# Optimization experiments

Hardware: AMD Instinct MI355X
Metric: run time of the kernel (lower is better)

Reference implementation:

```python
import jax, jax.numpy as jnp
import numpy as np

B, T, H, L = 64, 1024, 1024, 2


def setup_inputs() -> dict:
    key = jax.random.key(0)
    ks = jax.random.split(key, 5)
    stdv = 1.0 / np.sqrt(H)
    u = lambda k, shape: jax.random.uniform(k, shape, jnp.float32, -stdv, stdv)
    return {
        "Xt": jax.random.normal(ks[0], (B, T, H), jnp.float32),
        "Wih": u(ks[1], (L, H, H)),
        "bih": u(ks[2], (L, H)),
        "Whh": u(ks[3], (L, H, H)),
        "bhh": u(ks[4], (L, H)),
    }


def reference(Xt, Wih, bih, Whh, bhh):
    # Stacked Elman RNN, batch_first, zero initial hidden state, tanh, dropout=0.
    # h: [L, B, H] stacked per-layer hidden states.
    h0 = jnp.zeros((L, B, H), Xt.dtype)

    def step(h, x_t):  # h: [L,B,H], x_t: [B,H]
        x = x_t
        new_h = []
        for i in range(L):
            x = jnp.tanh(x @ Wih[i].T + bih[i] + h[i] @ Whh[i].T + bhh[i])
            new_h.append(x)
        return jnp.stack(new_h), x  # carry new hidden, emit top-layer output

    xs = jnp.swapaxes(Xt, 0, 1)  # [T, B, H]
    hT, ys = jax.lax.scan(step, h0, xs)
    out = jnp.swapaxes(ys, 0, 1)  # [B, T, H]
    return (out, hT)
```

## Files before the change

kernel.cpp:

```cpp
#include <hip/hip_runtime.h>
#include <hip/hip_bf16.h>
#include <stdint.h>

#define HH 1024
#define BB 64
#define TT 1024

typedef __attribute__((ext_vector_type(8))) short short8;
typedef __attribute__((ext_vector_type(4))) float f32x4;

__device__ __forceinline__ unsigned short f2bf(float f) {
  union { float f; unsigned u; } v; v.f = f;
  unsigned r = v.u + 0x7fffu + ((v.u >> 16) & 1u);
  return (unsigned short)(r >> 16);
}

__device__ __forceinline__ float h2f(unsigned short u) {
  _Float16 h;
  __builtin_memcpy(&h, &u, 2);
  return (float)h;
}

__device__ __forceinline__ float ftanh(float x) {
  float e = __expf(2.0f * x);
  return 1.0f - 2.0f * __builtin_amdgcn_rcpf(e + 1.0f);
}

__global__ void prep_kernel(const float* __restrict__ Wih, const float* __restrict__ Whh,
                            const float* __restrict__ bih, const float* __restrict__ bhh,
                            unsigned short* __restrict__ wih_b, unsigned short* __restrict__ whh_b,
                            float* __restrict__ bias01) {
  int i = blockIdx.x * 256 + threadIdx.x;
  wih_b[i] = f2bf(Wih[i]);
  whh_b[i] = f2bf(Whh[i]);
  if (i < 2 * HH) bias01[i] = bih[i] + bhh[i];
}

__device__ __forceinline__ size_t rowperm(int r) {
  return ((size_t)(r & 63) << 10) | (size_t)(r >> 6);
}

template<bool ABF16, bool APERM, bool CPERM, bool OUTF16>
__global__ __launch_bounds__(256)
void gemm_bias(const void* __restrict__ Av, const unsigned short* __restrict__ Wb,
               const float* __restrict__ bias, void* __restrict__ GoutV) {
  __shared__ unsigned short As[128 * 40];
  __shared__ unsigned short Bs[128 * 40];
  const int tn = blockIdx.x & 7;
  const int tm = blockIdx.x >> 3;
  const int tid = threadIdx.x;
  const int wid = tid >> 6, lane = tid & 63;
  const int wr = (wid >> 1) * 64, wc = (wid & 1) * 64;
  const int l15 = lane & 15, l4 = lane >> 4;
  f32x4 acc[4][4] = {};

  const float* Af = (const float*)Av;
  const unsigned short* Ab = (const unsigned short*)Av;
  const int sr = tid >> 2;
  const int sk = (tid & 3) * 8;

  for (int k0 = 0; k0 < HH; k0 += 32) {
    __syncthreads();
#pragma unroll
    for (int p = 0; p < 2; ++p) {
      const int row = p * 64 + sr;
      const int rg = tm * 128 + row;
      const size_t ar = APERM ? rowperm(rg) : (size_t)rg;
      if (ABF16) {
        const unsigned short* src = Ab + ar * HH + k0 + sk;
        *(short8*)&As[row * 40 + sk] = *(const short8*)src;
      } else {
        const float* src = Af + ar * HH + k0 + sk;
        float4 x = *(const float4*)src;
        float4 y = *(const float4*)(src + 4);
        short8 v;
        v[0] = (short)f2bf(x.x); v[1] = (short)f2bf(x.y);
        v[2] = (short)f2bf(x.z); v[3] = (short)f2bf(x.w);
        v[4] = (short)f2bf(y.x); v[5] = (short)f2bf(y.y);
        v[6] = (short)f2bf(y.z); v[7] = (short)f2bf(y.w);
        *(short8*)&As[row * 40 + sk] = v;
      }
      const unsigned short* wsrc = Wb + (size_t)(tn * 128 + row) * HH + k0 + sk;
      *(short8*)&Bs[row * 40 + sk] = *(const short8*)wsrc;
    }
    __syncthreads();
    short8 a[4], b[4];
#pragma unroll
    for (int i = 0; i < 4; ++i) a[i] = *(short8*)&As[(wr + i * 16 + l15) * 40 + l4 * 8];
#pragma unroll
    for (int j = 0; j < 4; ++j) b[j] = *(short8*)&Bs[(wc + j * 16 + l15) * 40 + l4 * 8];
#pragma unroll
    for (int i = 0; i < 4; ++i)
#pragma unroll
      for (int j = 0; j < 4; ++j)
        acc[i][j] = __builtin_amdgcn_mfma_f32_16x16x32_bf16(a[i], b[j], acc[i][j], 0, 0, 0);
  }
#pragma unroll
  for (int j = 0; j < 4; ++j) {
    const int gc = tn * 128 + wc + j * 16 + l15;
    const float bv = bias[gc];
#pragma unroll
    for (int i = 0; i < 4; ++i) {
#pragma unroll
      for (int jj = 0; jj < 4; ++jj) {
        const int gr = tm * 128 + wr + i * 16 + l4 * 4 + jj;
        const size_t orow = CPERM ? rowperm(gr) : (size_t)gr;
        const float val = acc[i][j][jj] + bv;
        if (OUTF16) ((_Float16*)GoutV)[orow * HH + gc] = (_Float16)val;
        else        ((float*)GoutV)[orow * HH + gc] = val;
      }
    }
  }
}

__global__ __launch_bounds__(256)
void rec_fused(const unsigned short* __restrict__ Gh,
               const unsigned short* __restrict__ Whh0_b,
               const unsigned short* __restrict__ Wih1_b,
               const unsigned short* __restrict__ Whh1_b,
               const float* __restrict__ bias1,
               unsigned short* __restrict__ h0p,
               unsigned short* __restrict__ h1p,
               float* __restrict__ outp,
               float* __restrict__ hT,
               unsigned int* flags) {
  const int g = blockIdx.x;
  const int tid = threadIdx.x, wid = tid >> 6, lane = tid & 63;
  const int l15 = lane & 15, l4 = lane >> 4, kp = l4 * 8;
  __shared__ unsigned short Wl0[16 * 1032];
  __shared__ unsigned short Wl1[16 * 2056];

  for (int idx = tid; idx < 16 * 64; idx += 256) {
    const int j = idx >> 6, kseg = (idx & 63) * 16;
    const short8* s0 = (const short8*)&Whh0_b[(size_t)(g * 16 + j) * HH + kseg];
    *(short8*)&Wl0[j * 1032 + kseg] = s0[0];
    *(short8*)&Wl0[j * 1032 + kseg + 8] = s0[1];
    const short8* s1 = (const short8*)&Wih1_b[(size_t)(g * 16 + j) * HH + kseg];
    *(short8*)&Wl1[j * 2056 + kseg] = s1[0];
    *(short8*)&Wl1[j * 2056 + kseg + 8] = s1[1];
    const short8* s2 = (const short8*)&Whh1_b[(size_t)(g * 16 + j) * HH + kseg];
    *(short8*)&Wl1[j * 2056 + 1024 + kseg] = s2[0];
    *(short8*)&Wl1[j * 2056 + 1024 + kseg + 8] = s2[1];
  }
  __syncthreads();

  const int col = g * 16 + l15;
  const unsigned short* b0row = &Wl0[l15 * 1032 + kp];
  const unsigned short* b1row = &Wl1[l15 * 2056 + kp];
  const float bc1 = bias1[col];
  const uint64_t myflag = (uint64_t)(flags + g);
  const uint64_t pollflag = (uint64_t)(flags + lane);

  int bidx[4];
#pragma unroll
  for (int jj = 0; jj < 4; ++jj) bidx[jj] = wid * 16 + l4 * 4 + jj;

  float gv[4], gn[4];
#pragma unroll
  for (int jj = 0; jj < 4; ++jj) gv[jj] = h2f(Gh[(size_t)bidx[jj] * HH + col]);

  for (int p = 0; p <= TT; ++p) {
    if (p + 1 < TT) {
#pragma unroll
      for (int jj = 0; jj < 4; ++jj)
        gn[jj] = h2f(Gh[((size_t)(p + 1) * BB + bidx[jj]) * HH + col]);
    }

    if (p < TT) {
      f32x4 acc0 = {}, acc1 = {};
      if (p > 0) {
        const unsigned short* arow =
            h0p + ((p - 1) & 1) * (BB * HH) + (size_t)(wid * 16 + l15) * HH + kp;
#pragma unroll
        for (int ks = 0; ks < 32; ks += 2) {
          short8 a0 = *(const short8*)(arow + ks * 32);
          short8 w0 = *(const short8*)(b0row + ks * 32);
          acc0 = __builtin_amdgcn_mfma_f32_16x16x32_bf16(a0, w0, acc0, 0, 0, 0);
          short8 a1 = *(const short8*)(arow + (ks + 1) * 32);
          short8 w1 = *(const short8*)(b0row + (ks + 1) * 32);
          acc1 = __builtin_amdgcn_mfma_f32_16x16x32_bf16(a1, w1, acc1, 0, 0, 0);
        }
      }
      unsigned short* hc = h0p + (p & 1) * (BB * HH);
#pragma unroll
      for (int jj = 0; jj < 4; ++jj) {
        const float pre = acc0[jj] + acc1[jj] + gv[jj];
        const float h = ftanh(pre);
        const unsigned short hb = f2bf(h);
        const uint64_t ha = (uint64_t)(hc + (size_t)bidx[jj] * HH + col);
        asm volatile("global_store_short %0, %1, off sc0 sc1"
                     :: "v"(ha), "v"((unsigned)hb) : "memory");
        if (p == TT - 1) hT[(size_t)bidx[jj] * HH + col] = h;
      }
    }

    if (p >= 1) {
      const int t1 = p - 1;
      f32x4 acc0 = {}, acc1 = {};
      {
        const unsigned short* arow =
            h0p + (t1 & 1) * (BB * HH) + (size_t)(wid * 16 + l15) * HH + kp;
#pragma unroll
        for (int ks = 0; ks < 32; ks += 2) {
          short8 a0 = *(const short8*)(arow + ks * 32);
          short8 w0 = *(const short8*)(b1row + ks * 32);
          acc0 = __builtin_amdgcn_mfma_f32_16x16x32_bf16(a0, w0, acc0, 0, 0, 0);
          short8 a1 = *(const short8*)(arow + (ks + 1) * 32);
          short8 w1 = *(const short8*)(b1row + (ks + 1) * 32);
          acc1 = __builtin_amdgcn_mfma_f32_16x16x32_bf16(a1, w1, acc1, 0, 0, 0);
        }
      }
      if (t1 > 0) {
        const unsigned short* arow =
            h1p + ((t1 - 1) & 1) * (BB * HH) + (size_t)(wid * 16 + l15) * HH + kp;
#pragma unroll
        for (int ks = 0; ks < 32; ks += 2) {
          short8 a0 = *(const short8*)(arow + ks * 32);
          short8 w0 = *(const short8*)(b1row + 1024 + ks * 32);
          acc0 = __builtin_amdgcn_mfma_f32_16x16x32_bf16(a0, w0, acc0, 0, 0, 0);
          short8 a1 = *(const short8*)(arow + (ks + 1) * 32);
          short8 w1 = *(const short8*)(b1row + 1024 + (ks + 1) * 32);
          acc1 = __builtin_amdgcn_mfma_f32_16x16x32_bf16(a1, w1, acc1, 0, 0, 0);
        }
      }
      unsigned short* hc = h1p + (t1 & 1) * (BB * HH);
#pragma unroll
      for (int jj = 0; jj < 4; ++jj) {
        const float pre = acc0[jj] + acc1[jj] + bc1;
        const float h = ftanh(pre);
        outp[((size_t)bidx[jj] * TT + t1) * HH + col] = h;
        if (t1 < TT - 1) {
          const unsigned short hb = f2bf(h);
          const uint64_t ha = (uint64_t)(hc + (size_t)bidx[jj] * HH + col);
          asm volatile("global_store_short %0, %1, off sc0 sc1"
                       :: "v"(ha), "v"((unsigned)hb) : "memory");
        } else {
          hT[BB * HH + (size_t)bidx[jj] * HH + col] = h;
        }
      }
    }

    if (p < TT) {
      asm volatile("s_waitcnt vmcnt(0)" ::: "memory");
      __syncthreads();
      if (tid == 0) {
        const unsigned val = (unsigned)(p + 1);
        asm volatile("s_waitcnt vmcnt(0)\n\t"
                     "global_store_dword %0, %1, off sc0 sc1"
                     :: "v"(myflag), "v"(val) : "memory");
      }
      if (wid == 0) {
        const unsigned tgt = (unsigned)(p + 1);
        unsigned v;
        do {
          asm volatile("global_load_dword %0, %1, off sc0 sc1\n\t"
                       "s_waitcnt vmcnt(0)"
                       : "=v"(v) : "v"(pollflag) : "memory");
        } while (!__all((int)(v >= tgt)));
        __builtin_amdgcn_fence(__ATOMIC_ACQUIRE, "agent");
      }
      __syncthreads();
#pragma unroll
      for (int jj = 0; jj < 4; ++jj) gv[jj] = gn[jj];
    }
  }
}

extern "C" void kernel_launch(void* const* d_in, const int* in_sizes, int n_in,
                              void* d_out, int out_size, void* d_ws, size_t ws_size,
                              hipStream_t stream) {
  const float* Xt  = (const float*)d_in[0];
  const float* Wih = (const float*)d_in[1];
  const float* bih = (const float*)d_in[2];
  const float* Whh = (const float*)d_in[3];
  const float* bhh = (const float*)d_in[4];
  float* out = (float*)d_out;
  float* hT  = out + (size_t)BB * TT * HH;

  char* ws = (char*)d_ws;
  unsigned short* wih_b  = (unsigned short*)(ws);
  unsigned short* whh_b  = (unsigned short*)(ws + (4u << 20));
  float*          bias01 = (float*)(ws + (8u << 20));
  unsigned short* Gh     = (unsigned short*)(ws + (16u << 20));
  unsigned short* h0p    = (unsigned short*)(ws + (145u << 20));
  unsigned short* h1p    = (unsigned short*)(ws + (146u << 20));
  unsigned int*   flags  = (unsigned int*)(ws + (147u << 20));

  if (ws_size < (150u << 20)) return;

  hipMemsetAsync(flags, 0, 4096, stream);
  prep_kernel<<<8192, 256, 0, stream>>>(Wih, Whh, bih, bhh, wih_b, whh_b, bias01);

  gemm_bias<false, true, false, true><<<4096, 256, 0, stream>>>(Xt, wih_b, bias01, Gh);

  {
    const unsigned short* G = Gh;
    const unsigned short* W0 = whh_b;
    const unsigned short* W1i = wih_b + (size_t)HH * HH;
    const unsigned short* W1h = whh_b + (size_t)HH * HH;
    const float* b1 = bias01 + HH;
    unsigned short* p0 = h0p;
    unsigned short* p1 = h1p;
    float* op = out;
    float* ht = hT;
    unsigned int* fl = flags;
    void* args[] = {&G, &W0, &W1i, &W1h, &b1, &p0, &p1, &op, &ht, &fl};
    hipLaunchCooperativeKernel((void*)rec_fused, dim3(64), dim3(256), args, 0, stream);
  }
}
```

Before: 16.19 ms.

## Replace persistent cooperative kernel with per-timestep kernel launches

Swaps the single cooperative persistent kernel and its flag-based grid barrier for 1025 separate step-kernel launches, so the kernel boundary serves as the inter-step synchronization. Each launch reloads the weight slices from global memory into LDS. Layer-1's input product is also merged into the layer-0 loop so both share the loaded h0 fragments. The trade is dropping the spin-wait barrier in exchange for per-launch overhead and repeated weight staging at every step.

```diff
diff --git a/kernel.cpp b/kernel.cpp
--- a/kernel.cpp
+++ b/kernel.cpp
@@ -114,16 +114,18 @@
 }
 
 __global__ __launch_bounds__(256)
-void rec_fused(const unsigned short* __restrict__ Gh,
-               const unsigned short* __restrict__ Whh0_b,
-               const unsigned short* __restrict__ Wih1_b,
-               const unsigned short* __restrict__ Whh1_b,
-               const float* __restrict__ bias1,
-               unsigned short* __restrict__ h0p,
-               unsigned short* __restrict__ h1p,
-               float* __restrict__ outp,
-               float* __restrict__ hT,
-               unsigned int* flags) {
+void step_kernel(int p,
+                 const unsigned short* __restrict__ Gh,
+                 const unsigned short* __restrict__ Whh0_b,
+                 const unsigned short* __restrict__ Wih1_b,
+                 const unsigned short* __restrict__ Whh1_b,
+                 const float* __restrict__ bias1,
+                 const unsigned short* __restrict__ h0_prev,
+                 unsigned short* __restrict__ h0_cur,
+                 const unsigned short* __restrict__ h1_prev,
+                 unsigned short* __restrict__ h1_cur,
+                 float* __restrict__ outp,
+                 float* __restrict__ hT) {
   const int g = blockIdx.x;
   const int tid = threadIdx.x, wid = tid >> 6, lane = tid & 63;
   const int l15 = lane & 15, l4 = lane >> 4, kp = l4 * 8;
@@ -132,136 +134,87 @@
 
   for (int idx = tid; idx < 16 * 64; idx += 256) {
     const int j = idx >> 6, kseg = (idx & 63) * 16;
-    const short8* s0 = (const short8*)&Whh0_b[(size_t)(g * 16 + j) * HH + kseg];
-    *(short8*)&Wl0[j * 1032 + kseg] = s0[0];
-    *(short8*)&Wl0[j * 1032 + kseg + 8] = s0[1];
-    const short8* s1 = (const short8*)&Wih1_b[(size_t)(g * 16 + j) * HH + kseg];
-    *(short8*)&Wl1[j * 2056 + kseg] = s1[0];
-    *(short8*)&Wl1[j * 2056 + kseg + 8] = s1[1];
-    const short8* s2 = (const short8*)&Whh1_b[(size_t)(g * 16 + j) * HH + kseg];
-    *(short8*)&Wl1[j * 2056 + 1024 + kseg] = s2[0];
-    *(short8*)&Wl1[j * 2056 + 1024 + kseg + 8] = s2[1];
+    if (p < TT) {
+      const short8* s0 = (const short8*)&Whh0_b[(size_t)(g * 16 + j) * HH + kseg];
+      *(short8*)&Wl0[j * 1032 + kseg] = s0[0];
+      *(short8*)&Wl0[j * 1032 + kseg + 8] = s0[1];
+    }
+    if (p >= 1) {
+      const short8* s1 = (const short8*)&Wih1_b[(size_t)(g * 16 + j) * HH + kseg];
+      *(short8*)&Wl1[j * 2056 + kseg] = s1[0];
+      *(short8*)&Wl1[j * 2056 + kseg + 8] = s1[1];
+      if (p >= 2) {
+        const short8* s2 = (const short8*)&Whh1_b[(size_t)(g * 16 + j) * HH + kseg];
+        *(short8*)&Wl1[j * 2056 + 1024 + kseg] = s2[0];
+        *(short8*)&Wl1[j * 2056 + 1024 + kseg + 8] = s2[1];
+      }
+    }
   }
   __syncthreads();
 
   const int col = g * 16 + l15;
   const unsigned short* b0row = &Wl0[l15 * 1032 + kp];
   const unsigned short* b1row = &Wl1[l15 * 2056 + kp];
-  const float bc1 = bias1[col];
-  const uint64_t myflag = (uint64_t)(flags + g);
-  const uint64_t pollflag = (uint64_t)(flags + lane);
+  const size_t arow_half = (size_t)(wid * 16 + l15) * HH + kp;
 
   int bidx[4];
 #pragma unroll
   for (int jj = 0; jj < 4; ++jj) bidx[jj] = wid * 16 + l4 * 4 + jj;
 
-  float gv[4], gn[4];
-#pragma unroll
-  for (int jj = 0; jj < 4; ++jj) gv[jj] = h2f(Gh[(size_t)bidx[jj] * HH + col]);
-
-  for (int p = 0; p <= TT; ++p) {
-    if (p + 1 < TT) {
-#pragma unroll
-      for (int jj = 0; jj < 4; ++jj)
-        gn[jj] = h2f(Gh[((size_t)(p + 1) * BB + bidx[jj]) * HH + col]);
-    }
-
-    if (p < TT) {
-      f32x4 acc0 = {}, acc1 = {};
-      if (p > 0) {
-        const unsigned short* arow =
-            h0p + ((p - 1) & 1) * (BB * HH) + (size_t)(wid * 16 + l15) * HH + kp;
-#pragma unroll
-        for (int ks = 0; ks < 32; ks += 2) {
-          short8 a0 = *(const short8*)(arow + ks * 32);
-          short8 w0 = *(const short8*)(b0row + ks * 32);
-          acc0 = __builtin_amdgcn_mfma_f32_16x16x32_bf16(a0, w0, acc0, 0, 0, 0);
-          short8 a1 = *(const short8*)(arow + (ks + 1) * 32);
-          short8 w1 = *(const short8*)(b0row + (ks + 1) * 32);
-          acc1 = __builtin_amdgcn_mfma_f32_16x16x32_bf16(a1, w1, acc1, 0, 0, 0);
-        }
-      }
-      unsigned short* hc = h0p + (p & 1) * (BB * HH);
-#pragma unroll
-      for (int jj = 0; jj < 4; ++jj) {
-        const float pre = acc0[jj] + acc1[jj] + gv[jj];
-        const float h = ftanh(pre);
-        const unsigned short hb = f2bf(h);
-        const uint64_t ha = (uint64_t)(hc + (size_t)bidx[jj] * HH + col);
-        asm volatile("global_store_short %0, %1, off sc0 sc1"
-                     :: "v"(ha), "v"((unsigned)hb) : "memory");
-        if (p == TT - 1) hT[(size_t)bidx[jj] * HH + col] = h;
-      }
-    }
-
-    if (p >= 1) {
-      const int t1 = p - 1;
-      f32x4 acc0 = {}, acc1 = {};
-      {
-        const unsigned short* arow =
-            h0p + (t1 & 1) * (BB * HH) + (size_t)(wid * 16 + l15) * HH + kp;
-#pragma unroll
-        for (int ks = 0; ks < 32; ks += 2) {
-          short8 a0 = *(const short8*)(arow + ks * 32);
-          short8 w0 = *(const short8*)(b1row + ks * 32);
-          acc0 = __builtin_amdgcn_mfma_f32_16x16x32_bf16(a0, w0, acc0, 0, 0, 0);
-          short8 a1 = *(const short8*)(arow + (ks + 1) * 32);
-          short8 w1 = *(const short8*)(b1row + (ks + 1) * 32);
-          acc1 = __builtin_amdgcn_mfma_f32_16x16x32_bf16(a1, w1, acc1, 0, 0, 0);
-        }
-      }
-      if (t1 > 0) {
-        const unsigned short* arow =
-            h1p + ((t1 - 1) & 1) * (BB * HH) + (size_t)(wid * 16 + l15) * HH + kp;
-#pragma unroll
-        for (int ks = 0; ks < 32; ks += 2) {
-          short8 a0 = *(const short8*)(arow + ks * 32);
-          short8 w0 = *(const short8*)(b1row + 1024 + ks * 32);
-          acc0 = __builtin_amdgcn_mfma_f32_16x16x32_bf16(a0, w0, acc0, 0, 0, 0);
-          short8 a1 = *(const short8*)(arow + (ks + 1) * 32);
-          short8 w1 = *(const short8*)(b1row + 1024 + (ks + 1) * 32);
-          acc1 = __builtin_amdgcn_mfma_f32_16x16x32_bf16(a1, w1, acc1, 0, 0, 0);
-        }
-      }
-      unsigned short* hc = h1p + (t1 & 1) * (BB * HH);
-#pragma unroll
-      for (int jj = 0; jj < 4; ++jj) {
-        const float pre = acc0[jj] + acc1[jj] + bc1;
-        const float h = ftanh(pre);
-        outp[((size_t)bidx[jj] * TT + t1) * HH + col] = h;
-        if (t1 < TT - 1) {
-          const unsigned short hb = f2bf(h);
-          const uint64_t ha = (uint64_t)(hc + (size_t)bidx[jj] * HH + col);
-          asm volatile("global_store_short %0, %1, off sc0 sc1"
-                       :: "v"(ha), "v"((unsigned)hb) : "memory");
-        } else {
-          hT[BB * HH + (size_t)bidx[jj] * HH + col] = h;
-        }
-      }
-    }
-
-    if (p < TT) {
-      asm volatile("s_waitcnt vmcnt(0)" ::: "memory");
-      __syncthreads();
-      if (tid == 0) {
-        const unsigned val = (unsigned)(p + 1);
-        asm volatile("s_waitcnt vmcnt(0)\n\t"
-                     "global_store_dword %0, %1, off sc0 sc1"
-                     :: "v"(myflag), "v"(val) : "memory");
-      }
-      if (wid == 0) {
-        const unsigned tgt = (unsigned)(p + 1);
-        unsigned v;
-        do {
-          asm volatile("global_load_dword %0, %1, off sc0 sc1\n\t"
-                       "s_waitcnt vmcnt(0)"
-                       : "=v"(v) : "v"(pollflag) : "memory");
-        } while (!__all((int)(v >= tgt)));
-        __builtin_amdgcn_fence(__ATOMIC_ACQUIRE, "agent");
-      }
-      __syncthreads();
-#pragma unroll
-      for (int jj = 0; jj < 4; ++jj) gv[jj] = gn[jj];
+  f32x4 c00 = {}, c01 = {}, cI0 = {}, cI1 = {};
+  if (p >= 1) {
+    const unsigned short* arow = h0_prev + arow_half;
+#pragma unroll
+    for (int ks = 0; ks < 32; ks += 2) {
+      short8 a0 = *(const short8*)(arow + ks * 32);
+      short8 a1 = *(const short8*)(arow + (ks + 1) * 32);
+      short8 wI0 = *(const short8*)(b1row + ks * 32);
+      short8 wI1 = *(const short8*)(b1row + (ks + 1) * 32);
+      cI0 = __builtin_amdgcn_mfma_f32_16x16x32_bf16(a0, wI0, cI0, 0, 0, 0);
+      cI1 = __builtin_amdgcn_mfma_f32_16x16x32_bf16(a1, wI1, cI1, 0, 0, 0);
+      if (p < TT) {
+        short8 w00 = *(const short8*)(b0row + ks * 32);
+        short8 w01 = *(const short8*)(b0row + (ks + 1) * 32);
+        c00 = __builtin_amdgcn_mfma_f32_16x16x32_bf16(a0, w00, c00, 0, 0, 0);
+        c01 = __builtin_amdgcn_mfma_f32_16x16x32_bf16(a1, w01, c01, 0, 0, 0);
+      }
+    }
+  }
+
+  if (p < TT) {
+#pragma unroll
+    for (int jj = 0; jj < 4; ++jj) {
+      const float gvv = h2f(Gh[((size_t)p * BB + bidx[jj]) * HH + col]);
+      const float pre = c00[jj] + c01[jj] + gvv;
+      const float h = ftanh(pre);
+      h0_cur[(size_t)bidx[jj] * HH + col] = f2bf(h);
+      if (p == TT - 1) hT[(size_t)bidx[jj] * HH + col] = h;
+    }
+  }
+
+  if (p >= 1) {
+    const int t1 = p - 1;
+    f32x4 cH0 = {}, cH1 = {};
+    if (t1 > 0) {
+      const unsigned short* arow = h1_prev + arow_half;
+#pragma unroll
+      for (int ks = 0; ks < 32; ks += 2) {
+        short8 a0 = *(const short8*)(arow + ks * 32);
+        short8 wH0 = *(const short8*)(b1row + 1024 + ks * 32);
+        cH0 = __builtin_amdgcn_mfma_f32_16x16x32_bf16(a0, wH0, cH0, 0, 0, 0);
+        short8 a1 = *(const short8*)(arow + (ks + 1) * 32);
+        short8 wH1 = *(const short8*)(b1row + 1024 + (ks + 1) * 32);
+        cH1 = __builtin_amdgcn_mfma_f32_16x16x32_bf16(a1, wH1, cH1, 0, 0, 0);
+      }
+    }
+    const float bc1 = bias1[col];
+#pragma unroll
+    for (int jj = 0; jj < 4; ++jj) {
+      const float pre = cI0[jj] + cI1[jj] + cH0[jj] + cH1[jj] + bc1;
+      const float h = ftanh(pre);
+      outp[((size_t)bidx[jj] * TT + t1) * HH + col] = h;
+      if (t1 < TT - 1) h1_cur[(size_t)bidx[jj] * HH + col] = f2bf(h);
+      else             hT[BB * HH + (size_t)bidx[jj] * HH + col] = h;
     }
   }
 }
@@ -284,27 +237,23 @@
   unsigned short* Gh     = (unsigned short*)(ws + (16u << 20));
   unsigned short* h0p    = (unsigned short*)(ws + (145u << 20));
   unsigned short* h1p    = (unsigned short*)(ws + (146u << 20));
-  unsigned int*   flags  = (unsigned int*)(ws + (147u << 20));
 
   if (ws_size < (150u << 20)) return;
 
-  hipMemsetAsync(flags, 0, 4096, stream);
   prep_kernel<<<8192, 256, 0, stream>>>(Wih, Whh, bih, bhh, wih_b, whh_b, bias01);
 
   gemm_bias<false, true, false, true><<<4096, 256, 0, stream>>>(Xt, wih_b, bias01, Gh);
 
-  {
-    const unsigned short* G = Gh;
-    const unsigned short* W0 = whh_b;
-    const unsigned short* W1i = wih_b + (size_t)HH * HH;
-    const unsigned short* W1h = whh_b + (size_t)HH * HH;
-    const float* b1 = bias01 + HH;
-    unsigned short* p0 = h0p;
-    unsigned short* p1 = h1p;
-    float* op = out;
-    float* ht = hT;
-    unsigned int* fl = flags;
-    void* args[] = {&G, &W0, &W1i, &W1h, &b1, &p0, &p1, &op, &ht, &fl};
-    hipLaunchCooperativeKernel((void*)rec_fused, dim3(64), dim3(256), args, 0, stream);
-  }
-}
+  const unsigned short* W1i = wih_b + (size_t)HH * HH;
+  const unsigned short* W1h = whh_b + (size_t)HH * HH;
+  const float* b1 = bias01 + HH;
+  const size_t BH = (size_t)BB * HH;
+  for (int p = 0; p <= TT; ++p) {
+    unsigned short* h0_prev = h0p + ((size_t)((p + 1) & 1)) * BH;
+    unsigned short* h0_cur  = h0p + ((size_t)(p & 1)) * BH;
+    unsigned short* h1_prev = h1p + ((size_t)(p & 1)) * BH;
+    unsigned short* h1_cur  = h1p + ((size_t)((p + 1) & 1)) * BH;
+    step_kernel<<<64, 256, 0, stream>>>(p, Gh, whh_b, W1i, W1h, b1,
+                                        h0_prev, h0_cur, h1_prev, h1_cur, out, hT);
+  }
+}
```

After: 16.09 ms. About the same (-0.7%).

## Stage hidden states into LDS and stream weights from global memory

Applied to the files above, without the earlier changes.

Weights are no longer kept resident in LDS. Instead, each step copies the previous layer-0 and layer-1 hidden states from global memory into LDS in two K-halves, using cache-bypassing vector loads, and the weight fragments are read straight from global memory (expected to stay in cache). The layer-0 and layer-1 input products now share one A-fragment read, and the acquire fence after polling is removed. This cuts the redundant per-wave global reads of the hidden state, but adds per-step staging plus extra barriers and puts weight reads on the global memory path. Dropping the fence relies on the sc0 sc1 loads for coherence.

```diff
diff --git a/kernel.cpp b/kernel.cpp
--- a/kernel.cpp
+++ b/kernel.cpp
@@ -5,9 +5,11 @@
 #define HH 1024
 #define BB 64
 #define TT 1024
+#define SST 520
 
 typedef __attribute__((ext_vector_type(8))) short short8;
 typedef __attribute__((ext_vector_type(4))) float f32x4;
+typedef __attribute__((ext_vector_type(4))) int i32x4;
 
 __device__ __forceinline__ unsigned short f2bf(float f) {
   union { float f; unsigned u; } v; v.f = f;
@@ -113,6 +115,26 @@
   }
 }
 
+__device__ __forceinline__ void stage_half(const unsigned short* src, int koff,
+                                           unsigned short* lds, int tid) {
+  i32x4 tmp[16];
+#pragma unroll
+  for (int i = 0; i < 16; ++i) {
+    const int linear = i * 256 + tid;
+    const int row = linear >> 6, c8 = linear & 63;
+    const uint64_t a = (uint64_t)(src + (size_t)row * HH + koff + c8 * 8);
+    asm volatile("global_load_dwordx4 %0, %1, off sc0 sc1" : "=&v"(tmp[i]) : "v"(a));
+  }
+  asm volatile("s_waitcnt vmcnt(0)" ::: "memory");
+  __builtin_amdgcn_sched_barrier(0);
+#pragma unroll
+  for (int i = 0; i < 16; ++i) {
+    const int linear = i * 256 + tid;
+    const int row = linear >> 6, c8 = linear & 63;
+    *(short8*)&lds[row * SST + c8 * 8] = __builtin_bit_cast(short8, tmp[i]);
+  }
+}
+
 __global__ __launch_bounds__(256)
 void rec_fused(const unsigned short* __restrict__ Gh,
                const unsigned short* __restrict__ Whh0_b,
@@ -127,26 +149,12 @@
   const int g = blockIdx.x;
   const int tid = threadIdx.x, wid = tid >> 6, lane = tid & 63;
   const int l15 = lane & 15, l4 = lane >> 4, kp = l4 * 8;
-  __shared__ unsigned short Wl0[16 * 1032];
-  __shared__ unsigned short Wl1[16 * 2056];
-
-  for (int idx = tid; idx < 16 * 64; idx += 256) {
-    const int j = idx >> 6, kseg = (idx & 63) * 16;
-    const short8* s0 = (const short8*)&Whh0_b[(size_t)(g * 16 + j) * HH + kseg];
-    *(short8*)&Wl0[j * 1032 + kseg] = s0[0];
-    *(short8*)&Wl0[j * 1032 + kseg + 8] = s0[1];
-    const short8* s1 = (const short8*)&Wih1_b[(size_t)(g * 16 + j) * HH + kseg];
-    *(short8*)&Wl1[j * 2056 + kseg] = s1[0];
-    *(short8*)&Wl1[j * 2056 + kseg + 8] = s1[1];
-    const short8* s2 = (const short8*)&Whh1_b[(size_t)(g * 16 + j) * HH + kseg];
-    *(short8*)&Wl1[j * 2056 + 1024 + kseg] = s2[0];
-    *(short8*)&Wl1[j * 2056 + 1024 + kseg + 8] = s2[1];
-  }
-  __syncthreads();
+  __shared__ unsigned short hs0[64 * SST];
+  __shared__ unsigned short hs1[64 * SST];
 
   const int col = g * 16 + l15;
-  const unsigned short* b0row = &Wl0[l15 * 1032 + kp];
-  const unsigned short* b1row = &Wl1[l15 * 2056 + kp];
+  const size_t wrow = (size_t)(g * 16 + l15) * HH;
+  const int r520 = (wid * 16 + l15) * SST;
   const float bc1 = bias1[col];
   const uint64_t myflag = (uint64_t)(flags + g);
   const uint64_t pollflag = (uint64_t)(flags + lane);
@@ -166,25 +174,52 @@
         gn[jj] = h2f(Gh[((size_t)(p + 1) * BB + bidx[jj]) * HH + col]);
     }
 
+    const unsigned short* h0_prev = h0p + ((p + 1) & 1) * (BB * HH);
+    const unsigned short* h1_prev = h1p + (p & 1) * (BB * HH);
+
+    f32x4 c00 = {}, c01 = {}, cI0 = {}, cI1 = {}, cH0 = {}, cH1 = {};
+
+#pragma unroll
+    for (int half = 0; half < 2; ++half) {
+      const int koff = half * 512;
+      if (half == 1) __syncthreads();
+      if (p >= 1) stage_half(h0_prev, koff, hs0, tid);
+      if (p >= 2) stage_half(h1_prev, koff, hs1, tid);
+      __syncthreads();
+
+      if (p >= 1) {
+#pragma unroll
+        for (int ks = 0; ks < 16; ks += 2) {
+          const int kk = ks * 32 + kp;
+          short8 a0 = *(const short8*)&hs0[r520 + kk];
+          short8 a1 = *(const short8*)&hs0[r520 + kk + 32];
+          short8 wI0 = *(const short8*)(Wih1_b + wrow + koff + kk);
+          short8 wI1 = *(const short8*)(Wih1_b + wrow + koff + kk + 32);
+          cI0 = __builtin_amdgcn_mfma_f32_16x16x32_bf16(a0, wI0, cI0, 0, 0, 0);
+          cI1 = __builtin_amdgcn_mfma_f32_16x16x32_bf16(a1, wI1, cI1, 0, 0, 0);
+          if (p < TT) {
+            short8 w00 = *(const short8*)(Whh0_b + wrow + koff + kk);
+            short8 w01 = *(const short8*)(Whh0_b + wrow + koff + kk + 32);
+            c00 = __builtin_amdgcn_mfma_f32_16x16x32_bf16(a0, w00, c00, 0, 0, 0);
+            c01 = __builtin_amdgcn_mfma_f32_16x16x32_bf16(a1, w01, c01, 0, 0, 0);
+          }
+          if (p >= 2) {
+            short8 b0 = *(const short8*)&hs1[r520 + kk];
+            short8 b1 = *(const short8*)&hs1[r520 + kk + 32];
+            short8 wH0 = *(const short8*)(Whh1_b + wrow + koff + kk);
+            short8 wH1 = *(const short8*)(Whh1_b + wrow + koff + kk + 32);
+            cH0 = __builtin_amdgcn_mfma_f32_16x16x32_bf16(b0, wH0, cH0, 0, 0, 0);
+            cH1 = __builtin_amdgcn_mfma_f32_16x16x32_bf16(b1, wH1, cH1, 0, 0, 0);
+          }
+        }
+      }
+    }
+
     if (p < TT) {
-      f32x4 acc0 = {}, acc1 = {};
-      if (p > 0) {
-        const unsigned short* arow =
-            h0p + ((p - 1) & 1) * (BB * HH) + (size_t)(wid * 16 + l15) * HH + kp;
-#pragma unroll
-        for (int ks = 0; ks < 32; ks += 2) {
-          short8 a0 = *(const short8*)(arow + ks * 32);
-          short8 w0 = *(const short8*)(b0row + ks * 32);
-          acc0 = __builtin_amdgcn_mfma_f32_16x16x32_bf16(a0, w0, acc0, 0, 0, 0);
-          short8 a1 = *(const short8*)(arow + (ks + 1) * 32);
-          short8 w1 = *(const short8*)(b0row + (ks + 1) * 32);
-          acc1 = __builtin_amdgcn_mfma_f32_16x16x32_bf16(a1, w1, acc1, 0, 0, 0);
-        }
-      }
       unsigned short* hc = h0p + (p & 1) * (BB * HH);
 #pragma unroll
       for (int jj = 0; jj < 4; ++jj) {
-        const float pre = acc0[jj] + acc1[jj] + gv[jj];
+        const float pre = c00[jj] + c01[jj] + gv[jj];
         const float h = ftanh(pre);
         const unsigned short hb = f2bf(h);
         const uint64_t ha = (uint64_t)(hc + (size_t)bidx[jj] * HH + col);
@@ -196,37 +231,10 @@
 
     if (p >= 1) {
       const int t1 = p - 1;
-      f32x4 acc0 = {}, acc1 = {};
-      {
-        const unsigned short* arow =
-            h0p + (t1 & 1) * (BB * HH) + (size_t)(wid * 16 + l15) * HH + kp;
-#pragma unroll
-        for (int ks = 0; ks < 32; ks += 2) {
-          short8 a0 = *(const short8*)(arow + ks * 32);
-          short8 w0 = *(const short8*)(b1row + ks * 32);
-          acc0 = __builtin_amdgcn_mfma_f32_16x16x32_bf16(a0, w0, acc0, 0, 0, 0);
-          short8 a1 = *(const short8*)(arow + (ks + 1) * 32);
-          short8 w1 = *(const short8*)(b1row + (ks + 1) * 32);
-          acc1 = __builtin_amdgcn_mfma_f32_16x16x32_bf16(a1, w1, acc1, 0, 0, 0);
-        }
-      }
-      if (t1 > 0) {
-        const unsigned short* arow =
-            h1p + ((t1 - 1) & 1) * (BB * HH) + (size_t)(wid * 16 + l15) * HH + kp;
-#pragma unroll
-        for (int ks = 0; ks < 32; ks += 2) {
-          short8 a0 = *(const short8*)(arow + ks * 32);
-          short8 w0 = *(const short8*)(b1row + 1024 + ks * 32);
-          acc0 = __builtin_amdgcn_mfma_f32_16x16x32_bf16(a0, w0, acc0, 0, 0, 0);
-          short8 a1 = *(const short8*)(arow + (ks + 1) * 32);
-          short8 w1 = *(const short8*)(b1row + 1024 + (ks + 1) * 32);
-          acc1 = __builtin_amdgcn_mfma_f32_16x16x32_bf16(a1, w1, acc1, 0, 0, 0);
-        }
-      }
       unsigned short* hc = h1p + (t1 & 1) * (BB * HH);
 #pragma unroll
       for (int jj = 0; jj < 4; ++jj) {
-        const float pre = acc0[jj] + acc1[jj] + bc1;
+        const float pre = cI0[jj] + cI1[jj] + cH0[jj] + cH1[jj] + bc1;
         const float h = ftanh(pre);
         outp[((size_t)bidx[jj] * TT + t1) * HH + col] = h;
         if (t1 < TT - 1) {
@@ -257,7 +265,6 @@
                        "s_waitcnt vmcnt(0)"
                        : "=v"(v) : "v"(pollflag) : "memory");
         } while (!__all((int)(v >= tgt)));
-        __builtin_amdgcn_fence(__ATOMIC_ACQUIRE, "agent");
       }
       __syncthreads();
 #pragma unroll
```

After: 19.71 ms. 1.22x slower.
